# Performance work log

Hardware: AMD Instinct MI355X
Metric: run time of the kernel (lower is better)

The kernel has to match this reference:

```python
import jax, jax.numpy as jnp
import numpy as np

# Similarity layer (simnets-tf), L2 similarity, ksize=3x3, stride 1, SAME padding,
# no normalization term, out_of_bounds_value = 0.
# sim[b,n,i,j] = -sum_{c,p,q} |w[n,c,p,q]| * (x_patch[b,c,i+p,j+q] - t[n,c,p,q])^2
# Expanded: -conv(x^2, |w|) + 2*conv(x, |w|*t) - sum(|w|*t^2)  (exact since pad value is 0).

B, C, H, W = 16, 64, 112, 112
N, KH, KW = 256, 3, 3
PAD = 1  # SAME padding for ksize 3


def _conv(inp, ker):
    # inp: [B,C,H',W'] padded, ker: [N,C,KH,KW] -> [B,N,H,W], VALID
    return jax.lax.conv_general_dilated(
        inp, ker, window_strides=(1, 1), padding='VALID',
        dimension_numbers=('NCHW', 'OIHW', 'NCHW'))


def setup_inputs() -> dict:
    key = jax.random.key(0)
    k1, k2, k3 = jax.random.split(key, 3)
    x = jax.random.normal(k1, (B, C, H, W), dtype=jnp.float32)
    sweights = jax.random.normal(k2, (N, C, KH, KW), dtype=jnp.float32)
    templates = jax.random.normal(k3, (N, C, KH, KW), dtype=jnp.float32)
    return {'x': x, 'sweights': sweights, 'templates': templates}


def reference(x, sweights, templates):
    w = jnp.abs(sweights)                      # layer applies tf.abs to weights
    xp = jnp.pad(x, ((0, 0), (0, 0), (PAD, PAD), (PAD, PAD)),
                 constant_values=0.0)          # out_of_bounds_value = 0
    sq_term = _conv(xp * xp, w)                # sum w * x^2 -> [B,N,H,W]
    cross = _conv(xp, w * templates)           # sum w * t * x
    const = jnp.sum(w * templates * templates, axis=(1, 2, 3))  # [N]
    return -sq_term + 2.0 * cross - const[None, :, None, None]
```

## Files before the change

kernel.cpp:

```cpp
#include <hip/hip_runtime.h>
#include <stdint.h>

#define B_ 16
#define C_ 64
#define H_ 112
#define W_ 112
#define N_ 256

typedef __attribute__((ext_vector_type(8))) short short8;
typedef __attribute__((ext_vector_type(4))) float floatx4;

typedef __attribute__((address_space(1))) const uint32_t gas_u32;
typedef __attribute__((address_space(3))) uint32_t las_u32;

__device__ __forceinline__ uint32_t f2bf_bits(float f) {
  uint32_t u = __float_as_uint(f);
  return (u + 0x7fffu + ((u >> 16) & 1u)) >> 16;
}

__global__ __launch_bounds__(256) void xform_x(const float* __restrict__ x,
                                               uint32_t* __restrict__ xq) {
  __shared__ float ls[64][113];
  int bi = blockIdx.x;
  int b = bi / H_, i = bi % H_;
  const float* xbase = x + ((size_t)b * C_) * (H_ * W_) + (size_t)i * W_;
  for (int idx = threadIdx.x; idx < C_ * 28; idx += 256) {
    int c = idx / 28, j4 = (idx - c * 28) * 4;
    float4 v = *(const float4*)(xbase + (size_t)c * (H_ * W_) + j4);
    ls[c][j4] = v.x;
    ls[c][j4 + 1] = v.y;
    ls[c][j4 + 2] = v.z;
    ls[c][j4 + 3] = v.w;
  }
  __syncthreads();
  uint32_t* orow = xq + ((size_t)(b * H_ + i)) * (W_ * C_);
  for (int idx = threadIdx.x; idx < W_ * 16; idx += 256) {
    int j = idx >> 4, c4 = (idx & 15) * 4;
    float a0 = ls[c4][j], a1 = ls[c4 + 1][j], a2 = ls[c4 + 2][j], a3 = ls[c4 + 3][j];
    uint4 o;
    o.x = f2bf_bits(a0) | (f2bf_bits(a0 * a0) << 16);
    o.y = f2bf_bits(a1) | (f2bf_bits(a1 * a1) << 16);
    o.z = f2bf_bits(a2) | (f2bf_bits(a2 * a2) << 16);
    o.w = f2bf_bits(a3) | (f2bf_bits(a3 * a3) << 16);
    *(uint4*)(orow + j * 64 + c4) = o;
  }
}

__global__ __launch_bounds__(64) void prep_wc(const float* __restrict__ sw,
                                              const float* __restrict__ tp,
                                              uint32_t* __restrict__ Wg,
                                              float* __restrict__ cN) {
  int n = blockIdx.x, c = threadIdx.x;
  int cg = c >> 5, kk = (c >> 4) & 1, ci = c & 15;
  const float* swp = sw + (size_t)(n * C_ + c) * 9;
  const float* tpp = tp + (size_t)(n * C_ + c) * 9;
  int sn = n >> 1;
  int cpos = ((n & 1) << 2) | (ci >> 2);
  int phys = sn * 32 + ((cpos ^ (sn & 7)) << 2) + (ci & 3);
  float s = 0.f;
#pragma unroll
  for (int tap = 0; tap < 9; ++tap) {
    float w = fabsf(swp[tap]);
    float t = tpp[tap];
    s += w * t * t;
    uint32_t v = f2bf_bits(2.0f * w * t) | (f2bf_bits(-w) << 16);
    Wg[(size_t)(cg * 18 + tap * 2 + kk) * 4096 + phys] = v;
  }
#pragma unroll
  for (int off = 32; off > 0; off >>= 1) s += __shfl_down(s, off);
  if (c == 0) cN[n] = s;
}

__global__ __launch_bounds__(512, 2) void sim_main(const uint32_t* __restrict__ xq,
                                                   const uint32_t* __restrict__ Wg,
                                                   const float* __restrict__ cN,
                                                   float* __restrict__ out) {
  extern __shared__ uint32_t smem[];
  uint32_t* xs = smem;
  uint32_t* ws = smem + 10368;

  int bx = blockIdx.x;
  int b = bx / 49;
  int rem = bx - b * 49;
  int rt = rem / 7, ct = rem - rt * 7;
  int r0 = rt * 16, c0 = ct * 16;
  int tid = threadIdx.x;
  int lane = tid & 63, wv = tid >> 6;
  int wn = wv & 1, wp = wv >> 1;
  int l15 = lane & 15, l4 = lane >> 4;

  floatx4 acc[8][4];
#pragma unroll
  for (int a = 0; a < 8; ++a)
#pragma unroll
    for (int p = 0; p < 4; ++p) acc[a][p] = (floatx4){0.f, 0.f, 0.f, 0.f};

  const uint32_t* xim = xq + (size_t)b * (H_ * W_ * C_);

  int afoff[8];
#pragma unroll
  for (int nt = 0; nt < 8; ++nt) {
    int n = wn * 128 + nt * 16 + l15;
    int sn = n >> 1;
    afoff[nt] = sn * 32 + (((((n & 1) << 2) | l4) ^ (sn & 7)) << 2);
  }

  auto stage_xs = [&](int cg) {
    for (int idx = tid; idx < 324 * 8; idx += 512) {
      int s = idx >> 3, ch = idx & 7;
      int row = s / 18, col = s - row * 18;
      int gi = r0 - 1 + row, gj = c0 - 1 + col;
      uint4 v = make_uint4(0u, 0u, 0u, 0u);
      if ((unsigned)gi < (unsigned)H_ && (unsigned)gj < (unsigned)W_)
        v = *(const uint4*)(xim + ((size_t)(gi * W_ + gj)) * C_ + cg * 32 + ch * 4);
      *(uint4*)(&xs[s * 32 + ((ch ^ (s & 7)) << 2)]) = v;
    }
  };
  auto stage_w = [&](int s) {
#pragma unroll
    for (int k = 0; k < 2; ++k) {
      const uint32_t* g = Wg + (size_t)s * 4096 + k * 2048 + wv * 256 + lane * 4;
      uint32_t* l = &ws[(s & 1) * 4096 + k * 2048 + wv * 256];
      __builtin_amdgcn_global_load_lds((gas_u32*)g, (las_u32*)l, 16, 0, 0);
    }
  };

  stage_xs(0);
  stage_w(0);
  __syncthreads();

#pragma unroll 1
  for (int s = 0; s < 36; ++s) {
    if (s == 18) {
      stage_xs(1);
      __syncthreads();
      stage_w(19);
    } else if (s < 35) {
      stage_w(s + 1);
    }
    int t2 = (s < 18) ? s : s - 18;
    int tap = t2 >> 1, kk = s & 1;
    int dp = tap / 3, dq = tap - dp * 3;
    const uint32_t* wsb = ws + (s & 1) * 4096;
    int chb = kk * 4 + l4;

    short8 bfr[4];
#pragma unroll
    for (int pt = 0; pt < 4; ++pt) {
      int st = (wp * 4 + pt + dp) * 18 + l15 + dq;
      bfr[pt] = *(const short8*)(&xs[st * 32 + ((chb ^ (st & 7)) << 2)]);
    }
    __builtin_amdgcn_s_setprio(1);
#pragma unroll
    for (int nt = 0; nt < 8; ++nt) {
      short8 af = *(const short8*)(wsb + afoff[nt]);
#pragma unroll
      for (int pt = 0; pt < 4; ++pt)
        acc[nt][pt] =
            __builtin_amdgcn_mfma_f32_16x16x32_bf16(af, bfr[pt], acc[nt][pt], 0, 0, 0);
    }
    __builtin_amdgcn_s_setprio(0);
    if (s < 35) __syncthreads();
  }

#pragma unroll
  for (int nt = 0; nt < 8; ++nt) {
#pragma unroll
    for (int v = 0; v < 4; ++v) {
      int n = wn * 128 + nt * 16 + l4 * 4 + v;
      float cv = cN[n];
#pragma unroll
      for (int pt = 0; pt < 4; ++pt) {
        int r = r0 + wp * 4 + pt;
        int col = c0 + l15;
        out[(((size_t)b * N_ + n) * H_ + r) * W_ + col] = acc[nt][pt][v] - cv;
      }
    }
  }
}

extern "C" void kernel_launch(void* const* d_in, const int* in_sizes, int n_in,
                              void* d_out, int out_size, void* d_ws, size_t ws_size,
                              hipStream_t stream) {
  const float* x = (const float*)d_in[0];
  const float* sw = (const float*)d_in[1];
  const float* tp = (const float*)d_in[2];
  float* out = (float*)d_out;

  const size_t xq_bytes = (size_t)B_ * H_ * W_ * C_ * 4;
  const size_t wg_bytes = (size_t)36 * 4096 * 4;
  uint32_t* xq = (uint32_t*)d_ws;
  uint32_t* Wg = (uint32_t*)((char*)d_ws + xq_bytes);
  float* cN = (float*)((char*)d_ws + xq_bytes + wg_bytes);

  const int smem_bytes = (10368 + 2 * 4096) * 4;
  static int smem_set = 0;
  if (!smem_set) {
    hipFuncSetAttribute((const void*)sim_main,
                        hipFuncAttributeMaxDynamicSharedMemorySize, smem_bytes);
    smem_set = 1;
  }

  xform_x<<<dim3(B_ * H_), dim3(256), 0, stream>>>(x, xq);
  prep_wc<<<dim3(N_), dim3(64), 0, stream>>>(sw, tp, Wg, cN);
  sim_main<<<dim3(B_ * 7 * 7), dim3(512), smem_bytes, stream>>>(xq, Wg, cN, out);
}
```

Baseline: 409.1 us.

## Software-pipeline MFMA loop with register double-buffering and 4-deep weight LDS ring

Both channel groups of the input tile are now staged into LDS up front, and the weight stages use a 4-slot ring instead of 2. The main loop is unrolled by two with ping-pong register fragments: fragments for the next step are loaded while MFMAs for the current step issue, and full __syncthreads are replaced by vmcnt waits plus raw barriers. The aim is to hide LDS load latency behind MFMA work and drop the mid-loop input restage stall. LDS use roughly doubles, to about 148 KB per block, which with __launch_bounds__(512,2) may limit occupancy to one block per CU, and register pressure rises from the extra fragment sets.

```diff
diff --git a/kernel.cpp b/kernel.cpp
--- a/kernel.cpp
+++ b/kernel.cpp
@@ -77,7 +77,7 @@
                                                    float* __restrict__ out) {
   extern __shared__ uint32_t smem[];
   uint32_t* xs = smem;
-  uint32_t* ws = smem + 10368;
+  uint32_t* ws = smem + 20736;
 
   int bx = blockIdx.x;
   int b = bx / 49;
@@ -97,13 +97,8 @@
 
   const uint32_t* xim = xq + (size_t)b * (H_ * W_ * C_);
 
-  int afoff[8];
-#pragma unroll
-  for (int nt = 0; nt < 8; ++nt) {
-    int n = wn * 128 + nt * 16 + l15;
-    int sn = n >> 1;
-    afoff[nt] = sn * 32 + (((((n & 1) << 2) | l4) ^ (sn & 7)) << 2);
-  }
+  int afb = wn * 2048 + (l15 >> 1) * 32 +
+            (((((l15 & 1) << 2) | l4) ^ ((l15 >> 1) & 7)) << 2);
 
   auto stage_xs = [&](int cg) {
     for (int idx = tid; idx < 324 * 8; idx += 512) {
@@ -113,55 +108,87 @@
       uint4 v = make_uint4(0u, 0u, 0u, 0u);
       if ((unsigned)gi < (unsigned)H_ && (unsigned)gj < (unsigned)W_)
         v = *(const uint4*)(xim + ((size_t)(gi * W_ + gj)) * C_ + cg * 32 + ch * 4);
-      *(uint4*)(&xs[s * 32 + ((ch ^ (s & 7)) << 2)]) = v;
+      *(uint4*)(&xs[cg * 10368 + s * 32 + ((ch ^ (s & 7)) << 2)]) = v;
     }
   };
   auto stage_w = [&](int s) {
 #pragma unroll
     for (int k = 0; k < 2; ++k) {
       const uint32_t* g = Wg + (size_t)s * 4096 + k * 2048 + wv * 256 + lane * 4;
-      uint32_t* l = &ws[(s & 1) * 4096 + k * 2048 + wv * 256];
+      uint32_t* l = &ws[(s & 3) * 4096 + k * 2048 + wv * 256];
       __builtin_amdgcn_global_load_lds((gas_u32*)g, (las_u32*)l, 16, 0, 0);
     }
   };
 
-  stage_xs(0);
-  stage_w(0);
-  __syncthreads();
-
-#pragma unroll 1
-  for (int s = 0; s < 36; ++s) {
-    if (s == 18) {
-      stage_xs(1);
-      __syncthreads();
-      stage_w(19);
-    } else if (s < 35) {
-      stage_w(s + 1);
-    }
+  auto loadf = [&](int s, short8* af, short8* bf) {
+    const uint32_t* wsb = ws + (s & 3) * 4096 + afb;
+#pragma unroll
+    for (int nt = 0; nt < 8; ++nt) af[nt] = *(const short8*)(wsb + nt * 256);
     int t2 = (s < 18) ? s : s - 18;
-    int tap = t2 >> 1, kk = s & 1;
+    int tap = t2 >> 1;
     int dp = tap / 3, dq = tap - dp * 3;
-    const uint32_t* wsb = ws + (s & 1) * 4096;
-    int chb = kk * 4 + l4;
-
-    short8 bfr[4];
+    int chb = ((s & 1) << 2) | l4;
+    const uint32_t* xb = xs + ((s < 18) ? 0 : 10368);
 #pragma unroll
     for (int pt = 0; pt < 4; ++pt) {
       int st = (wp * 4 + pt + dp) * 18 + l15 + dq;
-      bfr[pt] = *(const short8*)(&xs[st * 32 + ((chb ^ (st & 7)) << 2)]);
-    }
+      bf[pt] = *(const short8*)(xb + st * 32 + ((chb ^ (st & 7)) << 2));
+    }
+  };
+  auto domfma = [&](short8* af, short8* bf) {
     __builtin_amdgcn_s_setprio(1);
 #pragma unroll
-    for (int nt = 0; nt < 8; ++nt) {
-      short8 af = *(const short8*)(wsb + afoff[nt]);
+    for (int nt = 0; nt < 8; ++nt)
 #pragma unroll
       for (int pt = 0; pt < 4; ++pt)
         acc[nt][pt] =
-            __builtin_amdgcn_mfma_f32_16x16x32_bf16(af, bfr[pt], acc[nt][pt], 0, 0, 0);
-    }
+            __builtin_amdgcn_mfma_f32_16x16x32_bf16(af[nt], bf[pt], acc[nt][pt], 0, 0, 0);
     __builtin_amdgcn_s_setprio(0);
-    if (s < 35) __syncthreads();
-  }
+  };
+
+  stage_xs(0);
+  stage_xs(1);
+  stage_w(0);
+  stage_w(1);
+  __syncthreads();
+
+  short8 afA[8], bfA[4], afB[8], bfB[4];
+  loadf(0, afA, bfA);
+
+#pragma unroll 1
+  for (int ss = 0; ss < 16; ++ss) {
+    int s = ss * 2;
+    stage_w(s + 2);
+    asm volatile("s_waitcnt vmcnt(2)" ::: "memory");
+    __builtin_amdgcn_s_barrier();
+    __builtin_amdgcn_sched_barrier(0);
+    loadf(s + 1, afB, bfB);
+    domfma(afA, bfA);
+    stage_w(s + 3);
+    asm volatile("s_waitcnt vmcnt(2)" ::: "memory");
+    __builtin_amdgcn_s_barrier();
+    __builtin_amdgcn_sched_barrier(0);
+    loadf(s + 2, afA, bfA);
+    domfma(afB, bfB);
+  }
+  stage_w(34);
+  asm volatile("s_waitcnt vmcnt(2)" ::: "memory");
+  __builtin_amdgcn_s_barrier();
+  __builtin_amdgcn_sched_barrier(0);
+  loadf(33, afB, bfB);
+  domfma(afA, bfA);
+  stage_w(35);
+  asm volatile("s_waitcnt vmcnt(2)" ::: "memory");
+  __builtin_amdgcn_s_barrier();
+  __builtin_amdgcn_sched_barrier(0);
+  loadf(34, afA, bfA);
+  domfma(afB, bfB);
+  asm volatile("s_waitcnt vmcnt(0)" ::: "memory");
+  __builtin_amdgcn_s_barrier();
+  __builtin_amdgcn_sched_barrier(0);
+  loadf(35, afB, bfB);
+  domfma(afA, bfA);
+  domfma(afB, bfB);
 
 #pragma unroll
   for (int nt = 0; nt < 8; ++nt) {
@@ -193,7 +220,7 @@
   uint32_t* Wg = (uint32_t*)((char*)d_ws + xq_bytes);
   float* cN = (float*)((char*)d_ws + xq_bytes + wg_bytes);
 
-  const int smem_bytes = (10368 + 2 * 4096) * 4;
+  const int smem_bytes = (20736 + 4 * 4096) * 4;
   static int smem_set = 0;
   if (!smem_set) {
     hipFuncSetAttribute((const void*)sim_main,
```

After: 398.3 us. 2.6% less time.

## Split output channels across two blocks per tile to raise occupancy

Applied to the files above, without the earlier changes.

Each block now handles half the output channels (128 instead of 256), so the grid doubles and per-thread accumulators drop from 32 to 16 float4s. Launch bounds are raised to 4 blocks per SM. The weight pipeline now stages both k-halves of a tap in one step, halving the barrier count. In exchange the input tile is staged twice (once per channel half), and LDS use per block (about 74 KB) may cap how many blocks actually co-reside.

```diff
diff --git a/kernel.cpp b/kernel.cpp
--- a/kernel.cpp
+++ b/kernel.cpp
@@ -71,7 +71,7 @@
   if (c == 0) cN[n] = s;
 }
 
-__global__ __launch_bounds__(512, 2) void sim_main(const uint32_t* __restrict__ xq,
+__global__ __launch_bounds__(512, 4) void sim_main(const uint32_t* __restrict__ xq,
                                                    const uint32_t* __restrict__ Wg,
                                                    const float* __restrict__ cN,
                                                    float* __restrict__ out) {
@@ -80,6 +80,8 @@
   uint32_t* ws = smem + 10368;
 
   int bx = blockIdx.x;
+  int nb = bx & 1;
+  bx >>= 1;
   int b = bx / 49;
   int rem = bx - b * 49;
   int rt = rem / 7, ct = rem - rt * 7;
@@ -89,21 +91,16 @@
   int wn = wv & 1, wp = wv >> 1;
   int l15 = lane & 15, l4 = lane >> 4;
 
-  floatx4 acc[8][4];
-#pragma unroll
-  for (int a = 0; a < 8; ++a)
+  floatx4 acc[4][4];
+#pragma unroll
+  for (int a = 0; a < 4; ++a)
 #pragma unroll
     for (int p = 0; p < 4; ++p) acc[a][p] = (floatx4){0.f, 0.f, 0.f, 0.f};
 
   const uint32_t* xim = xq + (size_t)b * (H_ * W_ * C_);
 
-  int afoff[8];
-#pragma unroll
-  for (int nt = 0; nt < 8; ++nt) {
-    int n = wn * 128 + nt * 16 + l15;
-    int sn = n >> 1;
-    afoff[nt] = sn * 32 + (((((n & 1) << 2) | l4) ^ (sn & 7)) << 2);
-  }
+  int afb = wn * 1024 + (l15 >> 1) * 32 +
+            (((((l15 & 1) << 2) | l4) ^ ((l15 >> 1) & 7)) << 2);
 
   auto stage_xs = [&](int cg) {
     for (int idx = tid; idx < 324 * 8; idx += 512) {
@@ -116,11 +113,12 @@
       *(uint4*)(&xs[s * 32 + ((ch ^ (s & 7)) << 2)]) = v;
     }
   };
-  auto stage_w = [&](int s) {
+  auto stage_w = [&](int t) {
 #pragma unroll
     for (int k = 0; k < 2; ++k) {
-      const uint32_t* g = Wg + (size_t)s * 4096 + k * 2048 + wv * 256 + lane * 4;
-      uint32_t* l = &ws[(s & 1) * 4096 + k * 2048 + wv * 256];
+      const uint32_t* g =
+          Wg + (size_t)(t * 2 + k) * 4096 + nb * 2048 + wv * 256 + lane * 4;
+      uint32_t* l = &ws[(t & 1) * 4096 + k * 2048 + wv * 256];
       __builtin_amdgcn_global_load_lds((gas_u32*)g, (las_u32*)l, 16, 0, 0);
     }
   };
@@ -130,44 +128,43 @@
   __syncthreads();
 
 #pragma unroll 1
-  for (int s = 0; s < 36; ++s) {
-    if (s == 18) {
+  for (int t = 0; t < 18; ++t) {
+    if (t == 9) {
       stage_xs(1);
       __syncthreads();
-      stage_w(19);
-    } else if (s < 35) {
-      stage_w(s + 1);
-    }
-    int t2 = (s < 18) ? s : s - 18;
-    int tap = t2 >> 1, kk = s & 1;
+    }
+    if (t < 17) stage_w(t + 1);
+    int tap = (t < 9) ? t : t - 9;
     int dp = tap / 3, dq = tap - dp * 3;
-    const uint32_t* wsb = ws + (s & 1) * 4096;
-    int chb = kk * 4 + l4;
-
-    short8 bfr[4];
-#pragma unroll
-    for (int pt = 0; pt < 4; ++pt) {
-      int st = (wp * 4 + pt + dp) * 18 + l15 + dq;
-      bfr[pt] = *(const short8*)(&xs[st * 32 + ((chb ^ (st & 7)) << 2)]);
-    }
-    __builtin_amdgcn_s_setprio(1);
-#pragma unroll
-    for (int nt = 0; nt < 8; ++nt) {
-      short8 af = *(const short8*)(wsb + afoff[nt]);
-#pragma unroll
-      for (int pt = 0; pt < 4; ++pt)
-        acc[nt][pt] =
-            __builtin_amdgcn_mfma_f32_16x16x32_bf16(af, bfr[pt], acc[nt][pt], 0, 0, 0);
-    }
-    __builtin_amdgcn_s_setprio(0);
-    if (s < 35) __syncthreads();
-  }
-
-#pragma unroll
-  for (int nt = 0; nt < 8; ++nt) {
+    const uint32_t* slab = ws + (t & 1) * 4096;
+
+#pragma unroll
+    for (int kk = 0; kk < 2; ++kk) {
+      const uint32_t* wsb = slab + kk * 2048 + afb;
+      int chb = (kk << 2) | l4;
+      short8 af[4], bf[4];
+#pragma unroll
+      for (int nt = 0; nt < 4; ++nt) af[nt] = *(const short8*)(wsb + nt * 256);
+#pragma unroll
+      for (int pt = 0; pt < 4; ++pt) {
+        int st = (wp * 4 + pt + dp) * 18 + l15 + dq;
+        bf[pt] = *(const short8*)(&xs[st * 32 + ((chb ^ (st & 7)) << 2)]);
+      }
+#pragma unroll
+      for (int nt = 0; nt < 4; ++nt)
+#pragma unroll
+        for (int pt = 0; pt < 4; ++pt)
+          acc[nt][pt] =
+              __builtin_amdgcn_mfma_f32_16x16x32_bf16(af[nt], bf[pt], acc[nt][pt], 0, 0, 0);
+    }
+    if (t < 17) __syncthreads();
+  }
+
+#pragma unroll
+  for (int nt = 0; nt < 4; ++nt) {
 #pragma unroll
     for (int v = 0; v < 4; ++v) {
-      int n = wn * 128 + nt * 16 + l4 * 4 + v;
+      int n = nb * 128 + wn * 64 + nt * 16 + l4 * 4 + v;
       float cv = cN[n];
 #pragma unroll
       for (int pt = 0; pt < 4; ++pt) {
@@ -203,5 +200,5 @@
 
   xform_x<<<dim3(B_ * H_), dim3(256), 0, stream>>>(x, xq);
   prep_wc<<<dim3(N_), dim3(64), 0, stream>>>(sw, tp, Wg, cN);
-  sim_main<<<dim3(B_ * 7 * 7), dim3(512), smem_bytes, stream>>>(xq, Wg, cN, out);
-}
+  sim_main<<<dim3(2 * B_ * 7 * 7), dim3(512), smem_bytes, stream>>>(xq, Wg, cN, out);
+}
```

After: 352.6 us. 1.16x faster.
